# Kernel tuning notes

Hardware: AMD Instinct MI355X
Metric: run time of the kernel (lower is better)

## Reference

```python
import jax, jax.numpy as jnp
import numpy as np

B, N, C_IN, C_H, NUM_CLASSES, E = 2048, 64, 512, 128, 2, 1024


def setup_inputs() -> dict:
    key = jax.random.key(0)
    ks = jax.random.split(key, 6)
    x = jax.random.normal(ks[0], (B, N, C_IN), dtype=jnp.float32)
    edge_index = jax.random.randint(ks[1], (2, E), 0, N, dtype=jnp.int64)
    W1 = jax.random.normal(ks[2], (C_IN, C_H), dtype=jnp.float32) / np.sqrt(C_IN)
    b1 = jnp.zeros((C_H,), jnp.float32)
    W2 = jax.random.normal(ks[3], (C_H, C_H), dtype=jnp.float32) / np.sqrt(C_H)
    b2 = jnp.zeros((C_H,), jnp.float32)
    fcW = jax.random.normal(ks[4], (C_H * N, NUM_CLASSES), dtype=jnp.float32) / np.sqrt(C_H * N)
    fcb = jnp.zeros((NUM_CLASSES,), jnp.float32)
    return {"x": x, "edge_index": edge_index, "W1": W1, "b1": b1,
            "W2": W2, "b2": b2, "fcW": fcW, "fcb": fcb}


def gcn_conv(x, edge_index, W, b):
    # x: [B, N, C]; GCNConv with added self-loops and symmetric normalization:
    # out = D^-1/2 (A + I) D^-1/2 (x W) + b
    n = x.shape[1]
    loops = jnp.arange(n, dtype=edge_index.dtype)
    src = jnp.concatenate([edge_index[0], loops])  # [E+N]
    dst = jnp.concatenate([edge_index[1], loops])  # [E+N]
    deg = jnp.zeros((n,), x.dtype).at[dst].add(1.0)
    norm = jnp.where(deg > 0, jax.lax.rsqrt(jnp.maximum(deg, 1.0)), 0.0)
    h = x @ W  # [B, N, C_out]
    coef = (norm[src] * norm[dst])[None, :, None]  # [1, E+N, 1]
    msg = h[:, src, :] * coef  # gather on shared edge list, batched
    out = jnp.zeros_like(h).at[:, dst, :].add(msg)  # scatter-add aggregation
    return out + b


def reference(x, edge_index, W1, b1, W2, b2, fcW, fcb):
    h = jax.nn.relu(gcn_conv(x, edge_index, W1, b1))
    h = jax.nn.relu(gcn_conv(h, edge_index, W2, b2))
    h = h.reshape(h.shape[0], -1)  # [B, N*C_H]
    return h @ fcW + fcb  # [B, NUM_CLASSES]
```

## Files before the change

### kernel.cpp

```cpp
#include <hip/hip_runtime.h>
#include <cstddef>

#define NN   64
#define CIN  512
#define CH   128

typedef unsigned short ushort_t;
typedef __attribute__((ext_vector_type(8))) short bf16x8;
typedef __attribute__((ext_vector_type(4))) short bf16x4;
typedef __attribute__((ext_vector_type(4))) float f32x4;

__device__ __forceinline__ ushort_t f2bf(float f) {
    union { float f; unsigned u; } v; v.f = f;
    unsigned r = v.u + 0x7fffu + ((v.u >> 16) & 1u);
    return (ushort_t)(r >> 16);
}
__device__ __forceinline__ float bf2f(ushort_t b) {
    union { unsigned u; float f; } v; v.u = ((unsigned)b) << 16;
    return v.f;
}

__global__ __launch_bounds__(256) void prep_all(const int* __restrict__ ei, int E,
                                                const float* __restrict__ W1,
                                                const float* __restrict__ W2,
                                                ushort_t* __restrict__ Ah, ushort_t* __restrict__ Al,
                                                ushort_t* __restrict__ W1h,
                                                ushort_t* __restrict__ W2h) {
    const int t = threadIdx.x;
    if (blockIdx.x == 0) {
        __shared__ float sdeg[NN];
        __shared__ float snorm[NN];
        __shared__ float sA[NN * NN];
        if (t < NN) sdeg[t] = 0.f;
        for (int i = t; i < NN * NN; i += 256) sA[i] = 0.f;
        __syncthreads();
        for (int e = t; e < E; e += 256) atomicAdd(&sdeg[ei[E + e]], 1.0f);
        __syncthreads();
        if (t < NN) snorm[t] = rsqrtf(sdeg[t] + 1.0f);
        __syncthreads();
        for (int e = t; e < E; e += 256) {
            int s = ei[e], d = ei[E + e];
            atomicAdd(&sA[d * NN + s], snorm[s] * snorm[d]);
        }
        if (t < NN) atomicAdd(&sA[t * NN + t], snorm[t] * snorm[t]);
        __syncthreads();
        for (int i = t; i < NN * NN; i += 256) {
            float a = sA[i];
            ushort_t h = f2bf(a);
            Ah[i] = h;
            Al[i] = f2bf(a - bf2f(h));
        }
    } else {
        const int idx = (blockIdx.x - 1) * 256 + t;
        const int stride = 64 * 256;
        for (int i = idx; i < CIN * CH; i += stride) {
            int k = i / CH, c = i % CH;
            W1h[c * CIN + k] = f2bf(W1[i]);
        }
        for (int i = idx; i < CH * CH; i += stride) {
            int k = i / CH, c = i % CH;
            W2h[c * CH + k] = f2bf(W2[i]);
        }
    }
}

__global__ __launch_bounds__(256, 2) void fused_all(
    const float* __restrict__ x,
    const ushort_t* __restrict__ W1h,
    const ushort_t* __restrict__ Ah, const ushort_t* __restrict__ Al,
    const ushort_t* __restrict__ W2h,
    const float* __restrict__ b1, const float* __restrict__ b2,
    const float* __restrict__ fcW, const float* __restrict__ fcb,
    float* __restrict__ out)
{
    __shared__ ushort_t lds[32768];
    __shared__ float sred[16];

    const int t   = threadIdx.x;
    const int l   = t & 63;
    const int w   = t >> 6;
    const int lr  = l & 15;
    const int lk  = l >> 4;
    const int lr7 = lr & 7;
    const size_t rbase = (size_t)blockIdx.x * 128;

    const float* xp0 = x + (rbase + w * 32 + lr) * CIN + lk * 8;
    bf16x8 wreg[4];
    float4 xraw[2][2][2];

    #pragma unroll
    for (int rf = 0; rf < 2; ++rf) {
        const float* xp = xp0 + rf * 16 * CIN;
        xraw[rf][0][0] = *reinterpret_cast<const float4*>(xp);
        xraw[rf][0][1] = *reinterpret_cast<const float4*>(xp + 4);
        xraw[rf][1][0] = *reinterpret_cast<const float4*>(xp + 32);
        xraw[rf][1][1] = *reinterpret_cast<const float4*>(xp + 36);
    }
    #pragma unroll
    for (int u = 0; u < 4; ++u) {
        int q = u * 256 + t, c = q >> 3, g = q & 7;
        wreg[u] = *reinterpret_cast<const bf16x8*>(W1h + (size_t)c * CIN + g * 8);
    }
    #pragma unroll
    for (int u = 0; u < 4; ++u) {
        int q = u * 256 + t, c = q >> 3, g = q & 7;
        *reinterpret_cast<bf16x8*>(&lds[c * 64 + ((g ^ (c & 7)) << 3)]) = wreg[u];
    }
    __syncthreads();

    f32x4 acc[2][8];
    #pragma unroll
    for (int rf = 0; rf < 2; ++rf)
        #pragma unroll
        for (int ct = 0; ct < 8; ++ct)
            #pragma unroll
            for (int i = 0; i < 4; ++i) acc[rf][ct][i] = 0.f;

    for (int kc = 0; kc < 8; ++kc) {
        const ushort_t* sWh = &lds[(kc & 1) * 8192];

        bf16x8 xh[2][2];
        #pragma unroll
        for (int rf = 0; rf < 2; ++rf)
            #pragma unroll
            for (int ks = 0; ks < 2; ++ks) {
                const float xv[8] = {xraw[rf][ks][0].x, xraw[rf][ks][0].y,
                                     xraw[rf][ks][0].z, xraw[rf][ks][0].w,
                                     xraw[rf][ks][1].x, xraw[rf][ks][1].y,
                                     xraw[rf][ks][1].z, xraw[rf][ks][1].w};
                #pragma unroll
                for (int j = 0; j < 8; ++j)
                    xh[rf][ks][j] = (short)f2bf(xv[j]);
            }
        if (kc < 7) {
            #pragma unroll
            for (int rf = 0; rf < 2; ++rf) {
                const float* xp = xp0 + rf * 16 * CIN + (kc + 1) * 64;
                xraw[rf][0][0] = *reinterpret_cast<const float4*>(xp);
                xraw[rf][0][1] = *reinterpret_cast<const float4*>(xp + 4);
                xraw[rf][1][0] = *reinterpret_cast<const float4*>(xp + 32);
                xraw[rf][1][1] = *reinterpret_cast<const float4*>(xp + 36);
            }
            #pragma unroll
            for (int u = 0; u < 4; ++u) {
                int q = u * 256 + t, c = q >> 3, g = q & 7;
                wreg[u] = *reinterpret_cast<const bf16x8*>(W1h + (size_t)c * CIN + (kc + 1) * 64 + g * 8);
            }
        }
        #pragma unroll
        for (int ks = 0; ks < 2; ++ks) {
            const int swz = (((ks << 2) | lk) ^ lr7) << 3;
            #pragma unroll
            for (int ct = 0; ct < 8; ++ct) {
                const int c = ct * 16 + lr;
                bf16x8 wh = *reinterpret_cast<const bf16x8*>(&sWh[c * 64 + swz]);
                #pragma unroll
                for (int rf = 0; rf < 2; ++rf)
                    acc[rf][ct] = __builtin_amdgcn_mfma_f32_16x16x32_bf16(xh[rf][ks], wh, acc[rf][ct], 0, 0, 0);
            }
        }
        if (kc < 7) {
            const int nb = ((kc & 1) ^ 1) * 8192;
            #pragma unroll
            for (int u = 0; u < 4; ++u) {
                int q = u * 256 + t, c = q >> 3, g = q & 7;
                *reinterpret_cast<bf16x8*>(&lds[nb + c * 64 + ((g ^ (c & 7)) << 3)]) = wreg[u];
            }
        }
        __syncthreads();
    }


    #pragma unroll
    for (int rf = 0; rf < 2; ++rf) {
        const int grow = w * 32 + rf * 16 + lk * 4;
        const int qb   = grow >> 6;
        const int n0   = grow & 63;
        const int gn   = n0 >> 3, noff = n0 & 7;
        #pragma unroll
        for (int ct = 0; ct < 8; ++ct) {
            const int c = ct * 16 + lr;
            bf16x4 yv;
            #pragma unroll
            for (int r = 0; r < 4; ++r) yv[r] = (short)f2bf(acc[rf][ct][r]);
            *reinterpret_cast<bf16x4*>(&lds[qb * 8192 + c * 64 + ((gn ^ lr7) << 3) + noff]) = yv;
        }
    }
    __syncthreads();

    const int q = w >> 1;
    const int h = w & 1;
    ushort_t* sYtq = &lds[q * 8192];
    ushort_t* sH1q = &lds[16384 + q * 8192];

    bf16x8 ahf[2][2], alf[2][2];
    #pragma unroll
    for (int rf = 0; rf < 2; ++rf)
        #pragma unroll
        for (int ks = 0; ks < 2; ++ks) {
            const int nrow = h * 32 + rf * 16 + lr;
            const int ko = ks * 32 + lk * 8;
            ahf[rf][ks] = *reinterpret_cast<const bf16x8*>(Ah + nrow * NN + ko);
            alf[rf][ks] = *reinterpret_cast<const bf16x8*>(Al + nrow * NN + ko);
        }
    {
        f32x4 hacc[2][8];
        #pragma unroll
        for (int rf = 0; rf < 2; ++rf)
            #pragma unroll
            for (int ct = 0; ct < 8; ++ct)
                #pragma unroll
                for (int i = 0; i < 4; ++i) hacc[rf][ct][i] = 0.f;
        #pragma unroll
        for (int ks = 0; ks < 2; ++ks) {
            const int swz = (((ks << 2) | lk) ^ lr7) << 3;
            #pragma unroll
            for (int ct = 0; ct < 8; ++ct) {
                const int c = ct * 16 + lr;
                bf16x8 y = *reinterpret_cast<const bf16x8*>(&sYtq[c * 64 + swz]);
                #pragma unroll
                for (int rf = 0; rf < 2; ++rf) {
                    hacc[rf][ct] = __builtin_amdgcn_mfma_f32_16x16x32_bf16(ahf[rf][ks], y, hacc[rf][ct], 0, 0, 0);
                    hacc[rf][ct] = __builtin_amdgcn_mfma_f32_16x16x32_bf16(alf[rf][ks], y, hacc[rf][ct], 0, 0, 0);
                }
            }
        }
        #pragma unroll
        for (int rf = 0; rf < 2; ++rf)
            #pragma unroll
            for (int ct = 0; ct < 8; ++ct) {
                const int c = ct * 16 + lr;
                const int gc = c >> 3;
                const float bias = b1[c];
                #pragma unroll
                for (int r = 0; r < 4; ++r) {
                    const int n = h * 32 + rf * 16 + lk * 4 + r;
                    float v = fmaxf(hacc[rf][ct][r] + bias, 0.f);
                    sH1q[n * 128 + ((gc ^ (n & 7)) << 3) + (c & 7)] = f2bf(v);
                }
            }
    }
    __syncthreads();

    #pragma unroll
    for (int u = 0; u < 8; ++u) {
        int idx = u * 256 + t;
        int c = idx >> 4, g = idx & 15;
        *reinterpret_cast<bf16x8*>(&lds[c * 128 + ((g ^ (c & 7)) << 3)]) =
            *reinterpret_cast<const bf16x8*>(W2h + (size_t)c * CH + g * 8);
    }
    __syncthreads();

    f32x4 acc2[2][8];
    #pragma unroll
    for (int rf = 0; rf < 2; ++rf)
        #pragma unroll
        for (int ct = 0; ct < 8; ++ct)
            #pragma unroll
            for (int i = 0; i < 4; ++i) acc2[rf][ct][i] = 0.f;
    {
        bf16x8 hf[2][4];
        #pragma unroll
        for (int rf = 0; rf < 2; ++rf) {
            const int n = h * 32 + rf * 16 + lr;
            #pragma unroll
            for (int ks = 0; ks < 4; ++ks) {
                const int gh = ((ks << 2) | lk) ^ (n & 7);
                hf[rf][ks] = *reinterpret_cast<const bf16x8*>(&sH1q[n * 128 + (gh << 3)]);
            }
        }
        #pragma unroll
        for (int ct = 0; ct < 8; ++ct) {
            const int c = ct * 16 + lr;
            #pragma unroll
            for (int ks = 0; ks < 4; ++ks) {
                const int gw = ((ks << 2) | lk) ^ (c & 7);
                bf16x8 w2 = *reinterpret_cast<const bf16x8*>(&lds[c * 128 + (gw << 3)]);
                #pragma unroll
                for (int rf = 0; rf < 2; ++rf)
                    acc2[rf][ct] = __builtin_amdgcn_mfma_f32_16x16x32_bf16(hf[rf][ks], w2, acc2[rf][ct], 0, 0, 0);
            }
        }
    }
    __syncthreads();

    #pragma unroll
    for (int rf = 0; rf < 2; ++rf) {
        const int n0 = h * 32 + rf * 16 + lk * 4;
        const int gn = n0 >> 3, noff = n0 & 7;
        #pragma unroll
        for (int ct = 0; ct < 8; ++ct) {
            const int c = ct * 16 + lr;
            bf16x4 yv;
            #pragma unroll
            for (int r = 0; r < 4; ++r) yv[r] = (short)f2bf(acc2[rf][ct][r]);
            *reinterpret_cast<bf16x4*>(&sYtq[c * 64 + ((gn ^ lr7) << 3) + noff]) = yv;
        }
    }
    __syncthreads();

    float p0 = 0.f, p1 = 0.f;
    {
        f32x4 h2[2][8];
        #pragma unroll
        for (int rf = 0; rf < 2; ++rf)
            #pragma unroll
            for (int ct = 0; ct < 8; ++ct)
                #pragma unroll
                for (int i = 0; i < 4; ++i) h2[rf][ct][i] = 0.f;
        #pragma unroll
        for (int ks = 0; ks < 2; ++ks) {
            const int swz = (((ks << 2) | lk) ^ lr7) << 3;
            #pragma unroll
            for (int ct = 0; ct < 8; ++ct) {
                const int c = ct * 16 + lr;
                bf16x8 y = *reinterpret_cast<const bf16x8*>(&sYtq[c * 64 + swz]);
                #pragma unroll
                for (int rf = 0; rf < 2; ++rf) {
                    h2[rf][ct] = __builtin_amdgcn_mfma_f32_16x16x32_bf16(ahf[rf][ks], y, h2[rf][ct], 0, 0, 0);
                    h2[rf][ct] = __builtin_amdgcn_mfma_f32_16x16x32_bf16(alf[rf][ks], y, h2[rf][ct], 0, 0, 0);
                }
            }
        }
        #pragma unroll
        for (int rf = 0; rf < 2; ++rf)
            #pragma unroll
            for (int ct = 0; ct < 8; ++ct) {
                const int c = ct * 16 + lr;
                const float bias = b2[c];
                #pragma unroll
                for (int r = 0; r < 4; ++r) {
                    const int n = h * 32 + rf * 16 + lk * 4 + r;
                    float v = fmaxf(h2[rf][ct][r] + bias, 0.f);
                    const float2 fw = *reinterpret_cast<const float2*>(fcW + ((size_t)(n * CH + c)) * 2);
                    p0 = fmaf(v, fw.x, p0);
                    p1 = fmaf(v, fw.y, p1);
                }
            }
    }
    #pragma unroll
    for (int off = 32; off > 0; off >>= 1) {
        p0 += __shfl_down(p0, off);
        p1 += __shfl_down(p1, off);
    }
    if (l == 0) { sred[w * 2] = p0; sred[w * 2 + 1] = p1; }
    __syncthreads();
    if (t == 0) {
        const size_t bA = (size_t)blockIdx.x * 2;
        out[bA * 2 + 0]       = sred[0] + sred[2] + fcb[0];
        out[bA * 2 + 1]       = sred[1] + sred[3] + fcb[1];
        out[(bA + 1) * 2 + 0] = sred[4] + sred[6] + fcb[0];
        out[(bA + 1) * 2 + 1] = sred[5] + sred[7] + fcb[1];
    }
}

extern "C" void kernel_launch(void* const* d_in, const int* in_sizes, int n_in,
                              void* d_out, int out_size, void* d_ws, size_t ws_size,
                              hipStream_t stream) {
    const float* x   = (const float*)d_in[0];
    const int*   ei  = (const int*)d_in[1];
    const float* W1  = (const float*)d_in[2];
    const float* b1  = (const float*)d_in[3];
    const float* W2  = (const float*)d_in[4];
    const float* b2  = (const float*)d_in[5];
    const float* fcW = (const float*)d_in[6];
    const float* fcb = (const float*)d_in[7];
    float* outp = (float*)d_out;

    ushort_t* Ah  = (ushort_t*)d_ws;
    ushort_t* Al  = Ah + NN * NN;
    ushort_t* W1h = Al + NN * NN;
    ushort_t* W2h = W1h + CIN * CH;

    const int E  = in_sizes[1] / 2;
    const int Bn = in_sizes[0] / (NN * CIN);

    prep_all<<<65, 256, 0, stream>>>(ei, E, W1, W2, Ah, Al, W1h, W2h);
    fused_all<<<Bn / 2, 256, 0, stream>>>(x, W1h, Ah, Al, W2h,
                                          b1, b2, fcW, fcb, outp);
}
```

Measured before the change: 75.87 us.

## Stage W1 into LDS in two large halves instead of per-chunk double buffering

The per-k-chunk double-buffered W1 staging through registers is replaced by two phases. Each phase loads half of W1 (128x256 bf16, 64KB) directly into LDS and then runs four k-chunks of MFMA without barriers in between. This cuts the barrier count from eight to about three and drops the register staging for weights. In exchange the W1 loads are exposed at each phase start instead of overlapping with MFMA work.

```diff
diff --git a/kernel.cpp b/kernel.cpp
--- a/kernel.cpp
+++ b/kernel.cpp
@@ -85,7 +85,6 @@
     const size_t rbase = (size_t)blockIdx.x * 128;
 
     const float* xp0 = x + (rbase + w * 32 + lr) * CIN + lk * 8;
-    bf16x8 wreg[4];
     float4 xraw[2][2][2];
 
     #pragma unroll
@@ -96,17 +95,6 @@
         xraw[rf][1][0] = *reinterpret_cast<const float4*>(xp + 32);
         xraw[rf][1][1] = *reinterpret_cast<const float4*>(xp + 36);
     }
-    #pragma unroll
-    for (int u = 0; u < 4; ++u) {
-        int q = u * 256 + t, c = q >> 3, g = q & 7;
-        wreg[u] = *reinterpret_cast<const bf16x8*>(W1h + (size_t)c * CIN + g * 8);
-    }
-    #pragma unroll
-    for (int u = 0; u < 4; ++u) {
-        int q = u * 256 + t, c = q >> 3, g = q & 7;
-        *reinterpret_cast<bf16x8*>(&lds[c * 64 + ((g ^ (c & 7)) << 3)]) = wreg[u];
-    }
-    __syncthreads();
 
     f32x4 acc[2][8];
     #pragma unroll
@@ -116,59 +104,60 @@
             #pragma unroll
             for (int i = 0; i < 4; ++i) acc[rf][ct][i] = 0.f;
 
-    for (int kc = 0; kc < 8; ++kc) {
-        const ushort_t* sWh = &lds[(kc & 1) * 8192];
-
-        bf16x8 xh[2][2];
-        #pragma unroll
-        for (int rf = 0; rf < 2; ++rf)
+    #pragma unroll
+    for (int ph = 0; ph < 2; ++ph) {
+        if (ph) __syncthreads();
+        #pragma unroll
+        for (int u = 0; u < 16; ++u) {
+            int idx = u * 256 + t;
+            int c = idx >> 5, g = idx & 31;
+            int gs = (g & ~7) | ((g & 7) ^ (c & 7));
+            *reinterpret_cast<bf16x8*>(&lds[c * 256 + gs * 8]) =
+                *reinterpret_cast<const bf16x8*>(W1h + (size_t)c * CIN + ph * 256 + g * 8);
+        }
+        __syncthreads();
+
+        #pragma unroll
+        for (int kc = 0; kc < 4; ++kc) {
+            const int gc = ph * 4 + kc;
+            bf16x8 xh[2][2];
+            #pragma unroll
+            for (int rf = 0; rf < 2; ++rf)
+                #pragma unroll
+                for (int ks = 0; ks < 2; ++ks) {
+                    const float xv[8] = {xraw[rf][ks][0].x, xraw[rf][ks][0].y,
+                                         xraw[rf][ks][0].z, xraw[rf][ks][0].w,
+                                         xraw[rf][ks][1].x, xraw[rf][ks][1].y,
+                                         xraw[rf][ks][1].z, xraw[rf][ks][1].w};
+                    #pragma unroll
+                    for (int j = 0; j < 8; ++j)
+                        xh[rf][ks][j] = (short)f2bf(xv[j]);
+                }
+            if (gc < 7) {
+                #pragma unroll
+                for (int rf = 0; rf < 2; ++rf) {
+                    const float* xp = xp0 + rf * 16 * CIN + (gc + 1) * 64;
+                    xraw[rf][0][0] = *reinterpret_cast<const float4*>(xp);
+                    xraw[rf][0][1] = *reinterpret_cast<const float4*>(xp + 4);
+                    xraw[rf][1][0] = *reinterpret_cast<const float4*>(xp + 32);
+                    xraw[rf][1][1] = *reinterpret_cast<const float4*>(xp + 36);
+                }
+            }
             #pragma unroll
             for (int ks = 0; ks < 2; ++ks) {
-                const float xv[8] = {xraw[rf][ks][0].x, xraw[rf][ks][0].y,
-                                     xraw[rf][ks][0].z, xraw[rf][ks][0].w,
-                                     xraw[rf][ks][1].x, xraw[rf][ks][1].y,
-                                     xraw[rf][ks][1].z, xraw[rf][ks][1].w};
-                #pragma unroll
-                for (int j = 0; j < 8; ++j)
-                    xh[rf][ks][j] = (short)f2bf(xv[j]);
-            }
-        if (kc < 7) {
-            #pragma unroll
-            for (int rf = 0; rf < 2; ++rf) {
-                const float* xp = xp0 + rf * 16 * CIN + (kc + 1) * 64;
-                xraw[rf][0][0] = *reinterpret_cast<const float4*>(xp);
-                xraw[rf][0][1] = *reinterpret_cast<const float4*>(xp + 4);
-                xraw[rf][1][0] = *reinterpret_cast<const float4*>(xp + 32);
-                xraw[rf][1][1] = *reinterpret_cast<const float4*>(xp + 36);
-            }
-            #pragma unroll
-            for (int u = 0; u < 4; ++u) {
-                int q = u * 256 + t, c = q >> 3, g = q & 7;
-                wreg[u] = *reinterpret_cast<const bf16x8*>(W1h + (size_t)c * CIN + (kc + 1) * 64 + g * 8);
-            }
-        }
-        #pragma unroll
-        for (int ks = 0; ks < 2; ++ks) {
-            const int swz = (((ks << 2) | lk) ^ lr7) << 3;
-            #pragma unroll
-            for (int ct = 0; ct < 8; ++ct) {
-                const int c = ct * 16 + lr;
-                bf16x8 wh = *reinterpret_cast<const bf16x8*>(&sWh[c * 64 + swz]);
-                #pragma unroll
-                for (int rf = 0; rf < 2; ++rf)
-                    acc[rf][ct] = __builtin_amdgcn_mfma_f32_16x16x32_bf16(xh[rf][ks], wh, acc[rf][ct], 0, 0, 0);
-            }
-        }
-        if (kc < 7) {
-            const int nb = ((kc & 1) ^ 1) * 8192;
-            #pragma unroll
-            for (int u = 0; u < 4; ++u) {
-                int q = u * 256 + t, c = q >> 3, g = q & 7;
-                *reinterpret_cast<bf16x8*>(&lds[nb + c * 64 + ((g ^ (c & 7)) << 3)]) = wreg[u];
-            }
-        }
-        __syncthreads();
-    }
+                #pragma unroll
+                for (int ct = 0; ct < 8; ++ct) {
+                    const int c = ct * 16 + lr;
+                    const int gk = kc * 8 + (((ks << 2) | lk) ^ (c & 7));
+                    bf16x8 wh = *reinterpret_cast<const bf16x8*>(&lds[c * 256 + gk * 8]);
+                    #pragma unroll
+                    for (int rf = 0; rf < 2; ++rf)
+                        acc[rf][ct] = __builtin_amdgcn_mfma_f32_16x16x32_bf16(xh[rf][ks], wh, acc[rf][ct], 0, 0, 0);
+                }
+            }
+        }
+    }
+    __syncthreads();
 
 
     #pragma unroll
```

Measured after the change: 76.45 us. No clear change (+0.8%).
